# Optimization experiments

Hardware: AMD Instinct MI355X
Metric: run time of the kernel (lower is better)

The kernel has to match this reference:

```python
import jax, jax.numpy as jnp
import numpy as np

EOS_COEF = 0.25
NEG_FILL = -1000000.0


def move_lineup(pred_legal_mat, pred_quality_vec, target_legal_mat):
    """Vectorized equivalent of the serial torch move_lineup.

    Key insight: the 'word' encoding w = i + 64*j is a bijection on (i, j), so a
    target move word matches a predicted move word iff they occupy the SAME (i, j)
    cell.  torch.nonzero enumerates in row-major order, so the target index t_idx
    is the row-major rank among target ones, and p_idx is the row-major rank among
    predicted positives at the same cell.
    """
    B, Q = pred_quality_vec.shape
    N = 64 * 64
    t = (target_legal_mat == 1).reshape(B, N)           # [B, 4096] bool
    p = (pred_legal_mat > 0).reshape(B, N)              # [B, 4096] bool
    t_rank = jnp.cumsum(t.astype(jnp.int32), axis=1) - 1  # rank among targets
    p_rank = jnp.cumsum(p.astype(jnp.int32), axis=1) - 1  # rank among preds
    # original: match only if found in preds and p_idx < Q-1 (last slot reserved)
    valid = t & p & (p_rank < Q - 1) & (t_rank < Q)
    p_safe = jnp.clip(p_rank, 0, Q - 1)
    vals = jnp.take_along_axis(pred_quality_vec, p_safe, axis=1)  # [B, N]
    t_safe = jnp.where(valid, jnp.clip(t_rank, 0, Q - 1), Q - 1)
    rows = jnp.broadcast_to(jnp.arange(B)[:, None], (B, N))
    # scatter-max: valid ranks are unique per batch; invalid entries carry -inf
    lined = jnp.full((B, Q), NEG_FILL, pred_quality_vec.dtype)
    lined = lined.at[rows, t_safe].max(jnp.where(valid, vals, -jnp.inf))
    lined = lined.at[:, -1].set(pred_quality_vec[:, -1])
    match = jnp.zeros((B, Q), jnp.float32)
    match = match.at[rows, t_safe].max(valid.astype(jnp.float32))
    match = match.at[:, -1].set(1.0)
    return lined, match


def cross_entropy_gen(inp, target):
    # faithful to the torch version: sum over BATCH dim 0, mean over class dim
    lse = jax.scipy.special.logsumexp(inp, axis=1)                      # [B]
    tn = target / (jnp.sum(target, axis=1, keepdims=True) + 1e-10)      # [B, C]
    return jnp.mean(-jnp.sum(tn * (inp - lse[:, None]), axis=0))


def criterion(pred_legal_mat, pred_quality_vec, target_legal_mat, target_quality_vec):
    # ---- label_loss: weighted BCEWithLogits over the flattened legality map ----
    x = pred_legal_mat.reshape(-1)
    tflat = target_legal_mat.reshape(-1)
    w = jnp.where(tflat == 0, EOS_COEF, 1.0)
    bce = jnp.maximum(x, 0.0) - x * tflat + jnp.log1p(jnp.exp(-jnp.abs(x)))
    loss_labels = jnp.mean(w * bce)
    # ---- mse_score_loss ----
    lined, match = move_lineup(pred_legal_mat, pred_quality_vec, target_legal_mat)
    tq = target_quality_vec * match
    loss_ce = cross_entropy_gen(lined[:, :-1], tq[:, :-1])
    loss_mse = jnp.mean((lined[:, -1] - tq[:, -1]) ** 2)
    loss_score = loss_ce * 200.0 + loss_mse
    return jnp.stack([loss_labels, loss_score])


def setup_inputs() -> dict:
    key = jax.random.key(0)
    k1, k2, k3, k4 = jax.random.split(key, 4)
    B, Q = 4096, 256
    pred_legal_mat = jax.random.normal(k1, (B, 64, 64), jnp.float32) - 2.5
    pred_quality_vec = jax.random.normal(k2, (B, Q), jnp.float32)
    # ~33 legal target moves per board (chess-like sparsity), values in {0, 1}
    target_legal_mat = (jax.random.uniform(k3, (B, 64, 64)) < 0.008).astype(jnp.float32)
    target_quality_vec = jax.random.uniform(k4, (B, Q), jnp.float32)
    return {
        "pred_legal_mat": pred_legal_mat,
        "pred_quality_vec": pred_quality_vec,
        "target_legal_mat": target_legal_mat,
        "target_quality_vec": target_quality_vec,
    }


def reference(pred_legal_mat, pred_quality_vec, target_legal_mat, target_quality_vec):
    return criterion(pred_legal_mat, pred_quality_vec, target_legal_mat, target_quality_vec)
```

## Files before the change

### kernel.cpp

```cpp
#include <hip/hip_runtime.h>
#include <cstdint>
#include <cstddef>

#define NEG_FILL -1000000.0f

__device__ __forceinline__ void load16_to_lds(const float* g, float* l) {
    auto g1 = (const __attribute__((address_space(1))) void*)g;
    auto l3 = (__attribute__((address_space(3))) void*)(uint32_t)(uintptr_t)l;
    __builtin_amdgcn_global_load_lds(g1, l3, 16, 0, 0);
}

__global__ __launch_bounds__(256) void criterion_rows(
    const float* __restrict__ pred_legal,
    const float* __restrict__ pred_quality,
    const float* __restrict__ target_legal,
    const float* __restrict__ target_quality,
    float* __restrict__ partials, int B) {

    const int b    = blockIdx.x;
    const int tid  = threadIdx.x;
    const int lane = tid & 63;
    const int w    = tid >> 6;

    __shared__ __align__(16) float xs[4096];
    __shared__ __align__(16) float ts[4096];
    __shared__ float lined[256];
    __shared__ float matchv[256];
    __shared__ int   scnt_t[4], scnt_p[4];
    __shared__ float sbce[4];
    __shared__ int   sent[4][8];

    const float* __restrict__ xrow  = pred_legal     + (size_t)b * 4096;
    const float* __restrict__ trow  = target_legal   + (size_t)b * 4096;
    const float* __restrict__ pqrow = pred_quality   + (size_t)b * 256;
    const float* __restrict__ tqrow = target_quality + (size_t)b * 256;

    #pragma unroll
    for (int i = 0; i < 4; ++i) {
        const int off = w * 1024 + i * 256;
        load16_to_lds(xrow + off + lane * 4, &xs[off]);
        load16_to_lds(trow + off + lane * 4, &ts[off]);
    }
    lined[tid]  = NEG_FILL;
    matchv[tid] = 0.0f;
    __syncthreads();

    float bce = 0.0f;
    int t_run = 0, p_run = 0, nm = 0;

    #pragma unroll
    for (int seg = 0; seg < 4; ++seg) {
        const int base = w * 1024 + seg * 256 + lane * 4;
        const float4 x4 = *(const float4*)&xs[base];
        const float4 t4 = *(const float4*)&ts[base];
        const float xv[4] = {x4.x, x4.y, x4.z, x4.w};
        const float tv[4] = {t4.x, t4.y, t4.z, t4.w};

        uint64_t bt[4], bp[4];
        #pragma unroll
        for (int e = 0; e < 4; ++e) {
            const float x = xv[e], t = tv[e];
            const float a  = __builtin_fabsf(x);
            const float p2 = __builtin_amdgcn_exp2f(a * -1.44269504f);
            const float L  = __builtin_amdgcn_logf(1.0f + p2) * 0.69314718f;
            const float relu = fmaxf(x, 0.0f);
            const float wgt  = 0.25f + 0.75f * t;
            bce += wgt * (relu - x * t + L);
            bt[e] = __ballot(t == 1.0f);
            bp[e] = __ballot(x > 0.0f);
        }

        const uint64_t bm0 = bt[0] & bp[0], bm1 = bt[1] & bp[1];
        const uint64_t bm2 = bt[2] & bp[2], bm3 = bt[3] & bp[3];
        if ((bm0 | bm1 | bm2 | bm3) != 0ull) {
            const uint64_t bms[4] = {bm0, bm1, bm2, bm3};
            #pragma unroll
            for (int e = 0; e < 4; ++e) {
                uint64_t m = bms[e];
                while (m) {
                    const int j = (int)__builtin_ctzll(m);
                    m &= m - 1;
                    const uint64_t below = (j == 0) ? 0ull : ((~0ull) >> (64 - j));
                    int ltr = t_run, lpr = p_run;
                    #pragma unroll
                    for (int e2 = 0; e2 < 4; ++e2) {
                        ltr += (int)__popcll(bt[e2] & below);
                        lpr += (int)__popcll(bp[e2] & below);
                        if (e2 < e) {
                            ltr += (int)((bt[e2] >> j) & 1ull);
                            lpr += (int)((bp[e2] >> j) & 1ull);
                        }
                    }
                    if (ltr < 256 && lpr < 255 && nm < 8) {
                        if (lane == 0) sent[w][nm] = (ltr << 8) | lpr;
                        ++nm;
                    }
                }
            }
        }
        t_run += (int)(__popcll(bt[0]) + __popcll(bt[1])
                     + __popcll(bt[2]) + __popcll(bt[3]));
        p_run += (int)(__popcll(bp[0]) + __popcll(bp[1])
                     + __popcll(bp[2]) + __popcll(bp[3]));
    }

    #pragma unroll
    for (int off = 32; off > 0; off >>= 1)
        bce += __shfl_xor(bce, off, 64);
    if (lane == 0) {
        scnt_t[w] = t_run; scnt_p[w] = p_run; sbce[w] = bce;
    }
    __syncthreads();

    {
        int baseT = 0, baseP = 0;
        #pragma unroll
        for (int k = 0; k < 4; ++k)
            if (k < w) { baseT += scnt_t[k]; baseP += scnt_p[k]; }
        for (int i = 0; i < nm; ++i) {
            const int ent = sent[w][i];
            const int tr = baseT + (ent >> 8);
            const int pr = baseP + (ent & 0xFF);
            if (tr < 256 && pr < 255 && lane == 0) {
                lined[tr]  = pqrow[pr];
                matchv[tr] = 1.0f;
            }
        }
    }
    __syncthreads();

    if (w == 0) {
        float vs[4], tq[4];
        #pragma unroll
        for (int k = 0; k < 4; ++k) {
            const int c = k * 64 + lane;
            vs[k] = lined[c];
            tq[k] = tqrow[c] * matchv[c];
        }
        if (lane == 63) { vs[3] = -3.0e38f; tq[3] = 0.0f; }

        float m = fmaxf(fmaxf(vs[0], vs[1]), fmaxf(vs[2], vs[3]));
        #pragma unroll
        for (int off = 32; off > 0; off >>= 1)
            m = fmaxf(m, __shfl_xor(m, off, 64));

        float s1 = 0.0f, s2 = 0.0f, s3 = 0.0f;
        #pragma unroll
        for (int k = 0; k < 4; ++k) {
            s1 += __builtin_amdgcn_exp2f((vs[k] - m) * 1.44269504f);
            s2 += tq[k];
            s3 += tq[k] * vs[k];
        }
        #pragma unroll
        for (int off = 32; off > 0; off >>= 1) {
            s1 += __shfl_xor(s1, off, 64);
            s2 += __shfl_xor(s2, off, 64);
            s3 += __shfl_xor(s3, off, 64);
        }

        if (lane == 0) {
            const float s0   = (sbce[0] + sbce[1]) + (sbce[2] + sbce[3]);
            const float lse  = m + __builtin_amdgcn_logf(s1) * 0.69314718f;
            const float csum = -(s3 - lse * s2) / (s2 + 1e-10f);
            const float d    = pqrow[255] - tqrow[255];
            float4 o;
            o.x = s0; o.y = csum; o.z = d * d; o.w = 0.0f;
            *(float4*)(partials + (size_t)b * 4) = o;
        }
    }
}

__global__ __launch_bounds__(256) void finalize_kernel(
    const float* __restrict__ partials, float* __restrict__ out, int B) {
    const int tid = threadIdx.x;
    double s0 = 0.0, s1 = 0.0, s2 = 0.0;
    for (int r = tid; r < B; r += 256) {
        const float4 p = *(const float4*)(partials + (size_t)r * 4);
        s0 += (double)p.x; s1 += (double)p.y; s2 += (double)p.z;
    }
    #pragma unroll
    for (int off = 32; off > 0; off >>= 1) {
        s0 += __shfl_xor(s0, off, 64);
        s1 += __shfl_xor(s1, off, 64);
        s2 += __shfl_xor(s2, off, 64);
    }
    __shared__ double red[3][4];
    const int lane = tid & 63, w = tid >> 6;
    if (lane == 0) { red[0][w] = s0; red[1][w] = s1; red[2][w] = s2; }
    __syncthreads();
    if (tid == 0) {
        const double bs = red[0][0] + red[0][1] + red[0][2] + red[0][3];
        const double cs = red[1][0] + red[1][1] + red[1][2] + red[1][3];
        const double qs = red[2][0] + red[2][1] + red[2][2] + red[2][3];
        out[0] = (float)(bs / ((double)B * 4096.0));
        out[1] = (float)(200.0 * (cs / 255.0) + qs / (double)B);
    }
}

extern "C" void kernel_launch(void* const* d_in, const int* in_sizes, int n_in,
                              void* d_out, int out_size, void* d_ws, size_t ws_size,
                              hipStream_t stream) {
    const float* pred_legal     = (const float*)d_in[0];
    const float* pred_quality   = (const float*)d_in[1];
    const float* target_legal   = (const float*)d_in[2];
    const float* target_quality = (const float*)d_in[3];

    const int B = in_sizes[0] / 4096;

    float* partials = (float*)d_ws;

    criterion_rows<<<B, 256, 0, stream>>>(
        pred_legal, pred_quality, target_legal, target_quality, partials, B);
    finalize_kernel<<<1, 256, 0, stream>>>(partials, (float*)d_out, B);
}
```

Measured before the change: 159.0 us.

## Process one row per wavefront with register double-buffered loads, dropping LDS and barriers

Each wavefront now handles a whole batch row instead of four waves sharing one row. Row data is loaded straight from global memory into registers with a two-chunk double buffer instead of async global-to-LDS copies. Matches are written directly into per-lane registers, which removes the shared-memory staging, the cross-wave prefix combine and all block barriers. This cuts LDS use and synchronisation and should raise occupancy, at the cost of more registers per thread and a longer serial scan per wave.

```diff
diff --git a/kernel.cpp b/kernel.cpp
--- a/kernel.cpp
+++ b/kernel.cpp
@@ -3,12 +3,6 @@
 #include <cstddef>
 
 #define NEG_FILL -1000000.0f
-
-__device__ __forceinline__ void load16_to_lds(const float* g, float* l) {
-    auto g1 = (const __attribute__((address_space(1))) void*)g;
-    auto l3 = (__attribute__((address_space(3))) void*)(uint32_t)(uintptr_t)l;
-    __builtin_amdgcn_global_load_lds(g1, l3, 16, 0, 0);
-}
 
 __global__ __launch_bounds__(256) void criterion_rows(
     const float* __restrict__ pred_legal,
@@ -17,156 +11,138 @@
     const float* __restrict__ target_quality,
     float* __restrict__ partials, int B) {
 
-    const int b    = blockIdx.x;
     const int tid  = threadIdx.x;
     const int lane = tid & 63;
     const int w    = tid >> 6;
-
-    __shared__ __align__(16) float xs[4096];
-    __shared__ __align__(16) float ts[4096];
-    __shared__ float lined[256];
-    __shared__ float matchv[256];
-    __shared__ int   scnt_t[4], scnt_p[4];
-    __shared__ float sbce[4];
-    __shared__ int   sent[4][8];
+    const int b    = blockIdx.x * 4 + w;
+    if (b >= B) return;
 
     const float* __restrict__ xrow  = pred_legal     + (size_t)b * 4096;
     const float* __restrict__ trow  = target_legal   + (size_t)b * 4096;
     const float* __restrict__ pqrow = pred_quality   + (size_t)b * 256;
     const float* __restrict__ tqrow = target_quality + (size_t)b * 256;
 
-    #pragma unroll
-    for (int i = 0; i < 4; ++i) {
-        const int off = w * 1024 + i * 256;
-        load16_to_lds(xrow + off + lane * 4, &xs[off]);
-        load16_to_lds(trow + off + lane * 4, &ts[off]);
-    }
-    lined[tid]  = NEG_FILL;
-    matchv[tid] = 0.0f;
-    __syncthreads();
+    float vs0 = NEG_FILL, vs1 = NEG_FILL, vs2 = NEG_FILL, vs3 = NEG_FILL;
+    float mt0 = 0.0f, mt1 = 0.0f, mt2 = 0.0f, mt3 = 0.0f;
+    float bce = 0.0f;
+    int t_run = 0, p_run = 0;
 
-    float bce = 0.0f;
-    int t_run = 0, p_run = 0, nm = 0;
+    float4 xbuf[2][4], tbuf[2][4];
 
     #pragma unroll
-    for (int seg = 0; seg < 4; ++seg) {
-        const int base = w * 1024 + seg * 256 + lane * 4;
-        const float4 x4 = *(const float4*)&xs[base];
-        const float4 t4 = *(const float4*)&ts[base];
-        const float xv[4] = {x4.x, x4.y, x4.z, x4.w};
-        const float tv[4] = {t4.x, t4.y, t4.z, t4.w};
+    for (int s = 0; s < 4; ++s) {
+        const int base = s * 256 + lane * 4;
+        xbuf[0][s] = *(const float4*)&xrow[base];
+        tbuf[0][s] = *(const float4*)&trow[base];
+    }
 
-        uint64_t bt[4], bp[4];
+    #pragma unroll
+    for (int chunk = 0; chunk < 4; ++chunk) {
+        const int cur = chunk & 1;
+        const int nxt = cur ^ 1;
+        if (chunk < 3) {
+            #pragma unroll
+            for (int s = 0; s < 4; ++s) {
+                const int base = (chunk + 1) * 1024 + s * 256 + lane * 4;
+                xbuf[nxt][s] = *(const float4*)&xrow[base];
+                tbuf[nxt][s] = *(const float4*)&trow[base];
+            }
+        }
         #pragma unroll
-        for (int e = 0; e < 4; ++e) {
-            const float x = xv[e], t = tv[e];
-            const float a  = __builtin_fabsf(x);
-            const float p2 = __builtin_amdgcn_exp2f(a * -1.44269504f);
-            const float L  = __builtin_amdgcn_logf(1.0f + p2) * 0.69314718f;
-            const float relu = fmaxf(x, 0.0f);
-            const float wgt  = 0.25f + 0.75f * t;
-            bce += wgt * (relu - x * t + L);
-            bt[e] = __ballot(t == 1.0f);
-            bp[e] = __ballot(x > 0.0f);
-        }
-
-        const uint64_t bm0 = bt[0] & bp[0], bm1 = bt[1] & bp[1];
-        const uint64_t bm2 = bt[2] & bp[2], bm3 = bt[3] & bp[3];
-        if ((bm0 | bm1 | bm2 | bm3) != 0ull) {
-            const uint64_t bms[4] = {bm0, bm1, bm2, bm3};
+        for (int s = 0; s < 4; ++s) {
+            const float xv[4] = {xbuf[cur][s].x, xbuf[cur][s].y,
+                                 xbuf[cur][s].z, xbuf[cur][s].w};
+            const float tv[4] = {tbuf[cur][s].x, tbuf[cur][s].y,
+                                 tbuf[cur][s].z, tbuf[cur][s].w};
+            uint64_t bt[4], bp[4];
             #pragma unroll
             for (int e = 0; e < 4; ++e) {
-                uint64_t m = bms[e];
-                while (m) {
-                    const int j = (int)__builtin_ctzll(m);
-                    m &= m - 1;
-                    const uint64_t below = (j == 0) ? 0ull : ((~0ull) >> (64 - j));
-                    int ltr = t_run, lpr = p_run;
-                    #pragma unroll
-                    for (int e2 = 0; e2 < 4; ++e2) {
-                        ltr += (int)__popcll(bt[e2] & below);
-                        lpr += (int)__popcll(bp[e2] & below);
-                        if (e2 < e) {
-                            ltr += (int)((bt[e2] >> j) & 1ull);
-                            lpr += (int)((bp[e2] >> j) & 1ull);
+                const float x = xv[e], t = tv[e];
+                const float a  = __builtin_fabsf(x);
+                const float p2 = __builtin_amdgcn_exp2f(a * -1.44269504f);
+                const float L  = __builtin_amdgcn_logf(1.0f + p2) * 0.69314718f;
+                bce += (0.25f + 0.75f * t) * (fmaxf(x, 0.0f) - x * t + L);
+                bt[e] = __ballot(t == 1.0f);
+                bp[e] = __ballot(x > 0.0f);
+            }
+
+            const uint64_t bm0 = bt[0] & bp[0], bm1 = bt[1] & bp[1];
+            const uint64_t bm2 = bt[2] & bp[2], bm3 = bt[3] & bp[3];
+            if ((bm0 | bm1 | bm2 | bm3) != 0ull) {
+                const uint64_t bms[4] = {bm0, bm1, bm2, bm3};
+                #pragma unroll
+                for (int e = 0; e < 4; ++e) {
+                    uint64_t m = bms[e];
+                    while (m) {
+                        const int j = (int)__builtin_ctzll(m);
+                        m &= m - 1;
+                        const uint64_t below =
+                            (j == 0) ? 0ull : ((~0ull) >> (64 - j));
+                        int tr = t_run, pr = p_run;
+                        #pragma unroll
+                        for (int e2 = 0; e2 < 4; ++e2) {
+                            tr += (int)__popcll(bt[e2] & below);
+                            pr += (int)__popcll(bp[e2] & below);
+                            if (e2 < e) {
+                                tr += (int)((bt[e2] >> j) & 1ull);
+                                pr += (int)((bp[e2] >> j) & 1ull);
+                            }
                         }
-                    }
-                    if (ltr < 256 && lpr < 255 && nm < 8) {
-                        if (lane == 0) sent[w][nm] = (ltr << 8) | lpr;
-                        ++nm;
+                        if (tr < 256 && pr < 255) {
+                            const float v = pqrow[pr];
+                            if (lane == (tr & 63)) {
+                                const int k = tr >> 6;
+                                if      (k == 0) { vs0 = v; mt0 = 1.0f; }
+                                else if (k == 1) { vs1 = v; mt1 = 1.0f; }
+                                else if (k == 2) { vs2 = v; mt2 = 1.0f; }
+                                else             { vs3 = v; mt3 = 1.0f; }
+                            }
+                        }
                     }
                 }
             }
+            t_run += (int)(__popcll(bt[0]) + __popcll(bt[1])
+                         + __popcll(bt[2]) + __popcll(bt[3]));
+            p_run += (int)(__popcll(bp[0]) + __popcll(bp[1])
+                         + __popcll(bp[2]) + __popcll(bp[3]));
         }
-        t_run += (int)(__popcll(bt[0]) + __popcll(bt[1])
-                     + __popcll(bt[2]) + __popcll(bt[3]));
-        p_run += (int)(__popcll(bp[0]) + __popcll(bp[1])
-                     + __popcll(bp[2]) + __popcll(bp[3]));
     }
 
     #pragma unroll
     for (int off = 32; off > 0; off >>= 1)
         bce += __shfl_xor(bce, off, 64);
+
+    float tq0 = tqrow[lane]        * mt0;
+    float tq1 = tqrow[64  + lane]  * mt1;
+    float tq2 = tqrow[128 + lane]  * mt2;
+    float tq3 = tqrow[192 + lane]  * mt3;
+    if (lane == 63) { vs3 = -3.0e38f; tq3 = 0.0f; }
+
+    float mx = fmaxf(fmaxf(vs0, vs1), fmaxf(vs2, vs3));
+    #pragma unroll
+    for (int off = 32; off > 0; off >>= 1)
+        mx = fmaxf(mx, __shfl_xor(mx, off, 64));
+
+    float s1 = __builtin_amdgcn_exp2f((vs0 - mx) * 1.44269504f)
+             + __builtin_amdgcn_exp2f((vs1 - mx) * 1.44269504f)
+             + __builtin_amdgcn_exp2f((vs2 - mx) * 1.44269504f)
+             + __builtin_amdgcn_exp2f((vs3 - mx) * 1.44269504f);
+    float s2 = tq0 + tq1 + tq2 + tq3;
+    float s3 = tq0 * vs0 + tq1 * vs1 + tq2 * vs2 + tq3 * vs3;
+    #pragma unroll
+    for (int off = 32; off > 0; off >>= 1) {
+        s1 += __shfl_xor(s1, off, 64);
+        s2 += __shfl_xor(s2, off, 64);
+        s3 += __shfl_xor(s3, off, 64);
+    }
+
     if (lane == 0) {
-        scnt_t[w] = t_run; scnt_p[w] = p_run; sbce[w] = bce;
-    }
-    __syncthreads();
-
-    {
-        int baseT = 0, baseP = 0;
-        #pragma unroll
-        for (int k = 0; k < 4; ++k)
-            if (k < w) { baseT += scnt_t[k]; baseP += scnt_p[k]; }
-        for (int i = 0; i < nm; ++i) {
-            const int ent = sent[w][i];
-            const int tr = baseT + (ent >> 8);
-            const int pr = baseP + (ent & 0xFF);
-            if (tr < 256 && pr < 255 && lane == 0) {
-                lined[tr]  = pqrow[pr];
-                matchv[tr] = 1.0f;
-            }
-        }
-    }
-    __syncthreads();
-
-    if (w == 0) {
-        float vs[4], tq[4];
-        #pragma unroll
-        for (int k = 0; k < 4; ++k) {
-            const int c = k * 64 + lane;
-            vs[k] = lined[c];
-            tq[k] = tqrow[c] * matchv[c];
-        }
-        if (lane == 63) { vs[3] = -3.0e38f; tq[3] = 0.0f; }
-
-        float m = fmaxf(fmaxf(vs[0], vs[1]), fmaxf(vs[2], vs[3]));
-        #pragma unroll
-        for (int off = 32; off > 0; off >>= 1)
-            m = fmaxf(m, __shfl_xor(m, off, 64));
-
-        float s1 = 0.0f, s2 = 0.0f, s3 = 0.0f;
-        #pragma unroll
-        for (int k = 0; k < 4; ++k) {
-            s1 += __builtin_amdgcn_exp2f((vs[k] - m) * 1.44269504f);
-            s2 += tq[k];
-            s3 += tq[k] * vs[k];
-        }
-        #pragma unroll
-        for (int off = 32; off > 0; off >>= 1) {
-            s1 += __shfl_xor(s1, off, 64);
-            s2 += __shfl_xor(s2, off, 64);
-            s3 += __shfl_xor(s3, off, 64);
-        }
-
-        if (lane == 0) {
-            const float s0   = (sbce[0] + sbce[1]) + (sbce[2] + sbce[3]);
-            const float lse  = m + __builtin_amdgcn_logf(s1) * 0.69314718f;
-            const float csum = -(s3 - lse * s2) / (s2 + 1e-10f);
-            const float d    = pqrow[255] - tqrow[255];
-            float4 o;
-            o.x = s0; o.y = csum; o.z = d * d; o.w = 0.0f;
-            *(float4*)(partials + (size_t)b * 4) = o;
-        }
+        const float lse  = mx + __builtin_amdgcn_logf(s1) * 0.69314718f;
+        const float csum = -(s3 - lse * s2) / (s2 + 1e-10f);
+        const float d    = pqrow[255] - tqrow[255];
+        float4 o;
+        o.x = bce; o.y = csum; o.z = d * d; o.w = 0.0f;
+        *(float4*)(partials + (size_t)b * 4) = o;
     }
 }
 
@@ -209,7 +185,7 @@
 
     float* partials = (float*)d_ws;
 
-    criterion_rows<<<B, 256, 0, stream>>>(
+    criterion_rows<<<(B + 3) / 4, 256, 0, stream>>>(
         pred_legal, pred_quality, target_legal, target_quality, partials, B);
     finalize_kernel<<<1, 256, 0, stream>>>(partials, (float*)d_out, B);
 }
```

Result: slower. 164.3 us (+3.3%).

## Process two rows per block with register loads instead of LDS staging

Applied to the files above, without the earlier changes.

Each 256-thread block now handles two batch rows, with two waves per row each covering 2048 cells. The global-to-LDS async loads and the 32KB shared staging buffers are replaced by direct float4 register loads, and the second chunk is prefetched while the first is processed. This cuts LDS usage, which should allow more resident blocks per CU, and halves the block count. In exchange it uses more registers for the buffered data, and each wave runs a longer serial scan.

```diff
diff --git a/kernel.cpp b/kernel.cpp
--- a/kernel.cpp
+++ b/kernel.cpp
@@ -3,12 +3,6 @@
 #include <cstddef>
 
 #define NEG_FILL -1000000.0f
-
-__device__ __forceinline__ void load16_to_lds(const float* g, float* l) {
-    auto g1 = (const __attribute__((address_space(1))) void*)g;
-    auto l3 = (__attribute__((address_space(3))) void*)(uint32_t)(uintptr_t)l;
-    __builtin_amdgcn_global_load_lds(g1, l3, 16, 0, 0);
-}
 
 __global__ __launch_bounds__(256) void criterion_rows(
     const float* __restrict__ pred_legal,
@@ -17,91 +11,107 @@
     const float* __restrict__ target_quality,
     float* __restrict__ partials, int B) {
 
-    const int b    = blockIdx.x;
     const int tid  = threadIdx.x;
     const int lane = tid & 63;
     const int w    = tid >> 6;
-
-    __shared__ __align__(16) float xs[4096];
-    __shared__ __align__(16) float ts[4096];
-    __shared__ float lined[256];
-    __shared__ float matchv[256];
+    const int r    = w >> 1;
+    const int h    = w & 1;
+    const int b    = blockIdx.x * 2 + r;
+    const bool active = (b < B);
+
+    __shared__ float lined[2][256];
+    __shared__ float matchv[2][256];
     __shared__ int   scnt_t[4], scnt_p[4];
     __shared__ float sbce[4];
     __shared__ int   sent[4][8];
 
-    const float* __restrict__ xrow  = pred_legal     + (size_t)b * 4096;
-    const float* __restrict__ trow  = target_legal   + (size_t)b * 4096;
+    const float* __restrict__ xrow  = pred_legal   + (size_t)b * 4096 + h * 2048;
+    const float* __restrict__ trow  = target_legal + (size_t)b * 4096 + h * 2048;
     const float* __restrict__ pqrow = pred_quality   + (size_t)b * 256;
     const float* __restrict__ tqrow = target_quality + (size_t)b * 256;
 
-    #pragma unroll
-    for (int i = 0; i < 4; ++i) {
-        const int off = w * 1024 + i * 256;
-        load16_to_lds(xrow + off + lane * 4, &xs[off]);
-        load16_to_lds(trow + off + lane * 4, &ts[off]);
-    }
-    lined[tid]  = NEG_FILL;
-    matchv[tid] = 0.0f;
-    __syncthreads();
+    float4 xb[2][4], tb[2][4];
+    if (active) {
+        #pragma unroll
+        for (int s = 0; s < 4; ++s) {
+            const int base = s * 256 + lane * 4;
+            xb[0][s] = *(const float4*)&xrow[base];
+            tb[0][s] = *(const float4*)&trow[base];
+        }
+    }
+
+    ((float*)lined)[tid]        = NEG_FILL;
+    ((float*)lined)[tid + 256]  = NEG_FILL;
+    ((float*)matchv)[tid]       = 0.0f;
+    ((float*)matchv)[tid + 256] = 0.0f;
 
     float bce = 0.0f;
     int t_run = 0, p_run = 0, nm = 0;
 
-    #pragma unroll
-    for (int seg = 0; seg < 4; ++seg) {
-        const int base = w * 1024 + seg * 256 + lane * 4;
-        const float4 x4 = *(const float4*)&xs[base];
-        const float4 t4 = *(const float4*)&ts[base];
-        const float xv[4] = {x4.x, x4.y, x4.z, x4.w};
-        const float tv[4] = {t4.x, t4.y, t4.z, t4.w};
-
-        uint64_t bt[4], bp[4];
-        #pragma unroll
-        for (int e = 0; e < 4; ++e) {
-            const float x = xv[e], t = tv[e];
-            const float a  = __builtin_fabsf(x);
-            const float p2 = __builtin_amdgcn_exp2f(a * -1.44269504f);
-            const float L  = __builtin_amdgcn_logf(1.0f + p2) * 0.69314718f;
-            const float relu = fmaxf(x, 0.0f);
-            const float wgt  = 0.25f + 0.75f * t;
-            bce += wgt * (relu - x * t + L);
-            bt[e] = __ballot(t == 1.0f);
-            bp[e] = __ballot(x > 0.0f);
-        }
-
-        const uint64_t bm0 = bt[0] & bp[0], bm1 = bt[1] & bp[1];
-        const uint64_t bm2 = bt[2] & bp[2], bm3 = bt[3] & bp[3];
-        if ((bm0 | bm1 | bm2 | bm3) != 0ull) {
-            const uint64_t bms[4] = {bm0, bm1, bm2, bm3};
+    if (active) {
+        #pragma unroll
+        for (int chunk = 0; chunk < 2; ++chunk) {
+            if (chunk == 0) {
+                #pragma unroll
+                for (int s = 0; s < 4; ++s) {
+                    const int base = 1024 + s * 256 + lane * 4;
+                    xb[1][s] = *(const float4*)&xrow[base];
+                    tb[1][s] = *(const float4*)&trow[base];
+                }
+            }
             #pragma unroll
-            for (int e = 0; e < 4; ++e) {
-                uint64_t m = bms[e];
-                while (m) {
-                    const int j = (int)__builtin_ctzll(m);
-                    m &= m - 1;
-                    const uint64_t below = (j == 0) ? 0ull : ((~0ull) >> (64 - j));
-                    int ltr = t_run, lpr = p_run;
+            for (int s = 0; s < 4; ++s) {
+                const float xv[4] = {xb[chunk][s].x, xb[chunk][s].y,
+                                     xb[chunk][s].z, xb[chunk][s].w};
+                const float tv[4] = {tb[chunk][s].x, tb[chunk][s].y,
+                                     tb[chunk][s].z, tb[chunk][s].w};
+                uint64_t bt[4], bp[4];
+                #pragma unroll
+                for (int e = 0; e < 4; ++e) {
+                    const float x = xv[e], t = tv[e];
+                    const float a  = __builtin_fabsf(x);
+                    const float p2 = __builtin_amdgcn_exp2f(a * -1.44269504f);
+                    const float L  = __builtin_amdgcn_logf(1.0f + p2) * 0.69314718f;
+                    bce += (0.25f + 0.75f * t) * (fmaxf(x, 0.0f) - x * t + L);
+                    bt[e] = __ballot(t == 1.0f);
+                    bp[e] = __ballot(x > 0.0f);
+                }
+
+                const uint64_t bm0 = bt[0] & bp[0], bm1 = bt[1] & bp[1];
+                const uint64_t bm2 = bt[2] & bp[2], bm3 = bt[3] & bp[3];
+                if ((bm0 | bm1 | bm2 | bm3) != 0ull) {
+                    const uint64_t bms[4] = {bm0, bm1, bm2, bm3};
                     #pragma unroll
-                    for (int e2 = 0; e2 < 4; ++e2) {
-                        ltr += (int)__popcll(bt[e2] & below);
-                        lpr += (int)__popcll(bp[e2] & below);
-                        if (e2 < e) {
-                            ltr += (int)((bt[e2] >> j) & 1ull);
-                            lpr += (int)((bp[e2] >> j) & 1ull);
+                    for (int e = 0; e < 4; ++e) {
+                        uint64_t m = bms[e];
+                        while (m) {
+                            const int j = (int)__builtin_ctzll(m);
+                            m &= m - 1;
+                            const uint64_t below =
+                                (j == 0) ? 0ull : ((~0ull) >> (64 - j));
+                            int ltr = t_run, lpr = p_run;
+                            #pragma unroll
+                            for (int e2 = 0; e2 < 4; ++e2) {
+                                ltr += (int)__popcll(bt[e2] & below);
+                                lpr += (int)__popcll(bp[e2] & below);
+                                if (e2 < e) {
+                                    ltr += (int)((bt[e2] >> j) & 1ull);
+                                    lpr += (int)((bp[e2] >> j) & 1ull);
+                                }
+                            }
+                            if (ltr < 256 && lpr < 255 && nm < 8) {
+                                if (lane == 0) sent[w][nm] = (ltr << 8) | lpr;
+                                ++nm;
+                            }
                         }
                     }
-                    if (ltr < 256 && lpr < 255 && nm < 8) {
-                        if (lane == 0) sent[w][nm] = (ltr << 8) | lpr;
-                        ++nm;
-                    }
                 }
+                t_run += (int)(__popcll(bt[0]) + __popcll(bt[1])
+                             + __popcll(bt[2]) + __popcll(bt[3]));
+                p_run += (int)(__popcll(bp[0]) + __popcll(bp[1])
+                             + __popcll(bp[2]) + __popcll(bp[3]));
             }
         }
-        t_run += (int)(__popcll(bt[0]) + __popcll(bt[1])
-                     + __popcll(bt[2]) + __popcll(bt[3]));
-        p_run += (int)(__popcll(bp[0]) + __popcll(bp[1])
-                     + __popcll(bp[2]) + __popcll(bp[3]));
     }
 
     #pragma unroll
@@ -112,42 +122,40 @@
     }
     __syncthreads();
 
-    {
-        int baseT = 0, baseP = 0;
-        #pragma unroll
-        for (int k = 0; k < 4; ++k)
-            if (k < w) { baseT += scnt_t[k]; baseP += scnt_p[k]; }
+    if (active) {
+        const int baseT = h ? scnt_t[w - 1] : 0;
+        const int baseP = h ? scnt_p[w - 1] : 0;
         for (int i = 0; i < nm; ++i) {
             const int ent = sent[w][i];
             const int tr = baseT + (ent >> 8);
             const int pr = baseP + (ent & 0xFF);
             if (tr < 256 && pr < 255 && lane == 0) {
-                lined[tr]  = pqrow[pr];
-                matchv[tr] = 1.0f;
+                lined[r][tr]  = pqrow[pr];
+                matchv[r][tr] = 1.0f;
             }
         }
     }
     __syncthreads();
 
-    if (w == 0) {
+    if (active && h == 0) {
         float vs[4], tq[4];
         #pragma unroll
         for (int k = 0; k < 4; ++k) {
             const int c = k * 64 + lane;
-            vs[k] = lined[c];
-            tq[k] = tqrow[c] * matchv[c];
+            vs[k] = lined[r][c];
+            tq[k] = tqrow[c] * matchv[r][c];
         }
         if (lane == 63) { vs[3] = -3.0e38f; tq[3] = 0.0f; }
 
-        float m = fmaxf(fmaxf(vs[0], vs[1]), fmaxf(vs[2], vs[3]));
+        float mx = fmaxf(fmaxf(vs[0], vs[1]), fmaxf(vs[2], vs[3]));
         #pragma unroll
         for (int off = 32; off > 0; off >>= 1)
-            m = fmaxf(m, __shfl_xor(m, off, 64));
+            mx = fmaxf(mx, __shfl_xor(mx, off, 64));
 
         float s1 = 0.0f, s2 = 0.0f, s3 = 0.0f;
         #pragma unroll
         for (int k = 0; k < 4; ++k) {
-            s1 += __builtin_amdgcn_exp2f((vs[k] - m) * 1.44269504f);
+            s1 += __builtin_amdgcn_exp2f((vs[k] - mx) * 1.44269504f);
             s2 += tq[k];
             s3 += tq[k] * vs[k];
         }
@@ -159,12 +167,12 @@
         }
 
         if (lane == 0) {
-            const float s0   = (sbce[0] + sbce[1]) + (sbce[2] + sbce[3]);
-            const float lse  = m + __builtin_amdgcn_logf(s1) * 0.69314718f;
+            const float bce_row = sbce[w] + sbce[w + 1];
+            const float lse  = mx + __builtin_amdgcn_logf(s1) * 0.69314718f;
             const float csum = -(s3 - lse * s2) / (s2 + 1e-10f);
             const float d    = pqrow[255] - tqrow[255];
             float4 o;
-            o.x = s0; o.y = csum; o.z = d * d; o.w = 0.0f;
+            o.x = bce_row; o.y = csum; o.z = d * d; o.w = 0.0f;
             *(float4*)(partials + (size_t)b * 4) = o;
         }
     }
@@ -209,7 +217,7 @@
 
     float* partials = (float*)d_ws;
 
-    criterion_rows<<<B, 256, 0, stream>>>(
+    criterion_rows<<<(B + 1) / 2, 256, 0, stream>>>(
         pred_legal, pred_quality, target_legal, target_quality, partials, B);
     finalize_kernel<<<1, 256, 0, stream>>>(partials, (float*)d_out, B);
 }
```

Result: no change. 161.7 us (+1.7%).
